# Kernel optimization log

Measured on AMD Instinct MI355X. Metric: run time of the kernel, lower is better.

Reference implementation:

```python
import jax, jax.numpy as jnp
import numpy as np


def _patches3x3(x):
    # x: [B,H,W,C] -> [B,H,W,9,C], SAME zero padding, patch index k = i*3+j
    B, H, W, C = x.shape
    p = jnp.pad(x, ((0, 0), (1, 1), (1, 1), (0, 0)))
    return jnp.stack([p[:, i:i + H, j:j + W, :] for i in range(3) for j in range(3)], axis=3)


def setup_inputs() -> dict:
    key = jax.random.key(0)
    k1, k2, k3 = jax.random.split(key, 3)
    B, H, W, CH, NC, DIM = 4, 80, 80, 256, 22, 256
    x = jax.random.normal(k1, (B, H, W, CH), dtype=jnp.float32)
    seg_mask = jax.random.uniform(k2, (B, H, W, NC), dtype=jnp.float32)
    # he_uniform over receptive field ch*3*3
    lim = np.sqrt(6.0 / (CH * 9)).astype(np.float32)
    conv_w = jax.random.uniform(k3, (CH, 3, 3, DIM), dtype=jnp.float32, minval=-lim, maxval=lim)
    return {"x": x, "seg_mask": seg_mask, "conv_w": conv_w}


def reference(x, seg_mask, conv_w):
    B, H, W, CH = x.shape
    NC = seg_mask.shape[-1]
    DIM = conv_w.shape[-1]
    # patches of segmentation map: [B,H,W,9,NC]
    s_patch = _patches3x3(seg_mask)
    m = seg_mask[:, :, :, None, :]                       # [B,H,W,1,NC]
    s_max = jnp.max(m, axis=-1, keepdims=True)           # [B,H,W,1,1]
    # keep patch values only for the argmax class at the center pixel
    sel = jnp.sum(jnp.where(m == s_max, s_patch, 0.0), axis=-1)  # [B,H,W,9]
    cnt = jnp.sum((sel != 0.0).astype(jnp.float32), axis=-1, keepdims=True)  # [B,H,W,1]
    norm = jnp.where(cnt > 0, 9.0 / jnp.maximum(cnt, 1.0), 0.0)  # divide_no_nan(9, cnt)
    # per-channel 3x3 patch extraction of features (== depthwise conv with eye(9))
    xp = _patches3x3(x)                                  # [B,H,W,9,CH]
    xp = xp * sel[..., None]                             # mask-gated patches
    w = conv_w.reshape(CH, 9, DIM)
    out = jnp.einsum('bhwkc,ckd->bhwd', xp, w) * norm    # [B,H,W,DIM]
    return out
```

## Files before the change

kernel.cpp:

```cpp
#include <hip/hip_runtime.h>
#include <hip/hip_bf16.h>
#include <cstdint>

#define B_ 4
#define H_ 80
#define W_ 80
#define CH_ 256
#define NC_ 22
#define DIM_ 256
#define NPIX (B_*H_*W_)

typedef unsigned short ushort;
typedef __attribute__((ext_vector_type(8))) short short8;
typedef __attribute__((ext_vector_type(4))) float floatx4;

static __device__ inline ushort f2bf(float v) {
    __hip_bfloat16 h = __float2bfloat16(v);
    ushort r;
    __builtin_memcpy(&r, &h, 2);
    return r;
}
static __device__ inline unsigned pk2(float a, float b) {
    return (unsigned)f2bf(a) | ((unsigned)f2bf(b) << 16);
}

__global__ __launch_bounds__(64) void sel_kernel(const float* __restrict__ seg,
                                                 float* __restrict__ ssel)
{
    int m = blockIdx.x * 64 + threadIdx.x;
    if (m >= NPIX) return;
    int w = m % W_;
    int h = (m / W_) % H_;
    int b = m / (W_ * H_);

    const float2* c2 = (const float2*)(seg + (size_t)m * NC_);
    float cv[NC_];
    #pragma unroll
    for (int c = 0; c < NC_ / 2; ++c) { float2 v = c2[c]; cv[2*c] = v.x; cv[2*c+1] = v.y; }
    float mx = -1e30f;
    #pragma unroll
    for (int c = 0; c < NC_; ++c) mx = fmaxf(mx, cv[c]);

    float sel[9];
    int cnt = 0;
    #pragma unroll
    for (int k = 0; k < 9; ++k) {
        int i = k / 3, j = k % 3;
        int hh = h + i - 1, ww = w + j - 1;
        float s = 0.f;
        if (hh >= 0 && hh < H_ && ww >= 0 && ww < W_) {
            const float2* n2 = (const float2*)(seg + ((size_t)((b * H_ + hh) * W_ + ww)) * NC_);
            #pragma unroll
            for (int c = 0; c < NC_ / 2; ++c) {
                float2 v = n2[c];
                s += (cv[2*c]   == mx) ? v.x : 0.f;
                s += (cv[2*c+1] == mx) ? v.y : 0.f;
            }
        }
        sel[k] = s;
        cnt += (s != 0.f) ? 1 : 0;
    }
    float norm = (cnt > 0) ? 9.f / (float)cnt : 0.f;
    #pragma unroll
    for (int k = 0; k < 9; ++k)
        ssel[k * NPIX + m] = sel[k] * norm;
}

__global__ __launch_bounds__(256) void cvt_w(const float* __restrict__ cw,
                                             ushort* __restrict__ wbT)
{
    __shared__ ushort ls[32][260];
    const int k  = blockIdx.x / 8;
    const int c0 = (blockIdx.x % 8) * 32;
    const int c   = threadIdx.x >> 3;
    const int seg = threadIdx.x & 7;

    const float* src = cw + ((size_t)(c0 + c) * 9 + k) * DIM_ + seg * 32;
    #pragma unroll
    for (int e = 0; e < 32; e += 4) {
        float4 v = *(const float4*)(src + e);
        unsigned* dst = (unsigned*)&ls[c][seg * 32 + e];
        dst[0] = pk2(v.x, v.y);
        dst[1] = pk2(v.z, v.w);
    }
    __syncthreads();

    const int d = threadIdx.x;
    ushort tmp[32];
    #pragma unroll
    for (int cc = 0; cc < 32; ++cc) tmp[cc] = ls[cc][d];
    uint4 o[4];
    __builtin_memcpy(o, tmp, 64);
    uint4* dst = (uint4*)(wbT + ((size_t)k * 256 + d) * 256 + c0);
    dst[0] = o[0]; dst[1] = o[1]; dst[2] = o[2]; dst[3] = o[3];
}

__global__ __launch_bounds__(256) void cvt_x(const float* __restrict__ x,
                                             ushort* __restrict__ xb)
{
    size_t idx = ((size_t)blockIdx.x * 256 + threadIdx.x) * 8;
    const float4* s = (const float4*)(x + idx);
    float4 a = s[0], b = s[1];
    uint4 o = make_uint4(pk2(a.x, a.y), pk2(a.z, a.w), pk2(b.x, b.y), pk2(b.z, b.w));
    *(uint4*)(xb + idx) = o;
}

template<bool XB16>
__global__ __launch_bounds__(256, 3) void conv2(const float* __restrict__ x,
                                                const ushort* __restrict__ xb,
                                                const float* __restrict__ ssel,
                                                const ushort* __restrict__ wbT,
                                                float* __restrict__ out)
{
    __shared__ ushort xsA[2][80 * 136];
    __shared__ float  sl[9][80];

    const int tid  = threadIdx.x;
    const int lane = tid & 63;
    const int wv   = tid >> 6;
    const int ln   = lane & 15;
    const int quad = lane >> 4;
    const int rt   = blockIdx.x;
    const int b    = rt / H_;
    const int h    = rt % H_;
    const int d0   = blockIdx.y * 128;

    int qm[5], qc[5];
    #pragma unroll
    for (int r = 0; r < 5; ++r) {
        int q = tid + 256 * r;
        qm[r] = q >> 4;
        qc[r] = q & 15;
    }

    for (int t = tid; t < 9 * 80; t += 256) {
        int k = t / 80, m = t - k * 80;
        sl[k][m] = ssel[k * NPIX + rt * W_ + m];
    }

    floatx4 O[5][2];
    #pragma unroll
    for (int i = 0; i < 5; ++i)
        #pragma unroll
        for (int jn = 0; jn < 2; ++jn)
            O[i][jn] = (floatx4){0.f, 0.f, 0.f, 0.f};

    uint4  sg[5];
    float4 fa[5], fb[5];
    bool   ok[5];

    auto stage_load = [&](int nit) {
        const int i   = nit / 6;
        const int rem = nit % 6;
        const int cc  = (rem / 3) * 128;
        const int jj  = rem % 3;
        const int rr  = h + i - 1;
        const bool rowok = (rr >= 0) && (rr < H_);
        const int rsafe = rowok ? rr : h;
        #pragma unroll
        for (int r = 0; r < 5; ++r) {
            const int col = qm[r] + jj - 1;
            const bool v = rowok && (col >= 0) && (col < W_);
            ok[r] = v;
            const size_t gp = ((size_t)(b * H_ + rsafe) * W_ + (v ? col : 0));
            if (XB16) {
                sg[r] = *(const uint4*)(xb + gp * CH_ + cc + qc[r] * 8);
            } else {
                const float* f = x + gp * CH_ + cc + qc[r] * 8;
                fa[r] = *(const float4*)f;
                fb[r] = *(const float4*)(f + 4);
            }
        }
    };
    auto stage_write = [&](int nit) {
        ushort* bp = xsA[nit & 1];
        #pragma unroll
        for (int r = 0; r < 5; ++r) {
            uint4 v;
            if (XB16) {
                v = ok[r] ? sg[r] : make_uint4(0u, 0u, 0u, 0u);
            } else {
                v = ok[r] ? make_uint4(pk2(fa[r].x, fa[r].y), pk2(fa[r].z, fa[r].w),
                                       pk2(fb[r].x, fb[r].y), pk2(fb[r].z, fb[r].w))
                          : make_uint4(0u, 0u, 0u, 0u);
            }
            *(uint4*)&bp[qm[r] * 136 + qc[r] * 8] = v;
        }
    };

    short8 Breg[8];
    auto loadB = [&](int nit) {
        const int i   = nit / 6;
        const int rem = nit % 6;
        const int cc  = (rem / 3) * 128;
        const int jj  = rem % 3;
        const int k   = 3 * i + jj;
        #pragma unroll
        for (int kk = 0; kk < 4; ++kk)
            #pragma unroll
            for (int jn = 0; jn < 2; ++jn)
                Breg[kk * 2 + jn] = *(const short8*)(wbT
                    + ((size_t)k * 256 + d0 + wv * 32 + jn * 16 + ln) * 256
                    + cc + kk * 32 + quad * 8);
    };

    stage_load(0);
    stage_write(0);
    loadB(0);
    __syncthreads();

    #pragma unroll 2
    for (int it = 0; it < 18; ++it) {
        const int i   = it / 6;
        const int rem = it % 6;
        const int jj  = rem % 3;
        const int k   = 3 * i + jj;
        const ushort* bp = xsA[it & 1];

        if (it < 17) stage_load(it + 1);

        floatx4 P[5][2];
        #pragma unroll
        for (int im = 0; im < 5; ++im)
            #pragma unroll
            for (int jn = 0; jn < 2; ++jn)
                P[im][jn] = (floatx4){0.f, 0.f, 0.f, 0.f};

        #pragma unroll
        for (int kk = 0; kk < 4; ++kk) {
            short8 a[5];
            #pragma unroll
            for (int im = 0; im < 5; ++im)
                a[im] = *(const short8*)&bp[(im * 16 + ln) * 136 + kk * 32 + quad * 8];
            #pragma unroll
            for (int im = 0; im < 5; ++im)
                #pragma unroll
                for (int jn = 0; jn < 2; ++jn)
                    P[im][jn] = __builtin_amdgcn_mfma_f32_16x16x32_bf16(
                        a[im], Breg[kk * 2 + jn], P[im][jn], 0, 0, 0);
        }

        if (it < 17) stage_write(it + 1);
        if (it < 17) loadB(it + 1);

        #pragma unroll
        for (int im = 0; im < 5; ++im) {
            const float4 sv = *(const float4*)&sl[k][im * 16 + quad * 4];
            #pragma unroll
            for (int jn = 0; jn < 2; ++jn) {
                O[im][jn][0] += sv.x * P[im][jn][0];
                O[im][jn][1] += sv.y * P[im][jn][1];
                O[im][jn][2] += sv.z * P[im][jn][2];
                O[im][jn][3] += sv.w * P[im][jn][3];
            }
        }
        __syncthreads();
    }

    #pragma unroll
    for (int im = 0; im < 5; ++im) {
        #pragma unroll
        for (int jn = 0; jn < 2; ++jn) {
            const int dd = d0 + wv * 32 + jn * 16 + ln;
            #pragma unroll
            for (int r = 0; r < 4; ++r) {
                const int m = im * 16 + quad * 4 + r;
                out[((size_t)(rt * W_ + m)) * DIM_ + dd] = O[im][jn][r];
            }
        }
    }
}

extern "C" void kernel_launch(void* const* d_in, const int* in_sizes, int n_in,
                              void* d_out, int out_size, void* d_ws, size_t ws_size,
                              hipStream_t stream)
{
    const float* x   = (const float*)d_in[0];
    const float* seg = (const float*)d_in[1];
    const float* cw  = (const float*)d_in[2];
    float* out = (float*)d_out;

    float*  ssel = (float*)d_ws;
    ushort* wbT  = (ushort*)((char*)d_ws + 921600);
    ushort* xb   = (ushort*)((char*)d_ws + 921600 + 1179648);
    const size_t need = 921600u + 1179648u + 13107200u;

    sel_kernel<<<dim3((NPIX + 63) / 64), dim3(64), 0, stream>>>(seg, ssel);
    cvt_w<<<dim3(72), dim3(256), 0, stream>>>(cw, wbT);

    if (ws_size >= need) {
        cvt_x<<<dim3(NPIX * CH_ / (256 * 8)), dim3(256), 0, stream>>>(x, xb);
        conv2<true><<<dim3(B_ * H_, 2), dim3(256), 0, stream>>>(x, xb, ssel, wbT, out);
    } else {
        conv2<false><<<dim3(B_ * H_, 2), dim3(256), 0, stream>>>(x, nullptr, ssel, wbT, out);
    }
}
```

Measured before the change: 157.4 us.

## Fuse prep kernels, fold selection scale into A staging, retile waves 2x2

The separate sel, weight-convert and x-convert kernels are merged into one prep launch, and sel is now computed per (tap, pixel) thread with normalisation moved into the conv kernel. The conv kernel reads fp32 x directly, multiplies by the per-pixel selection weight while packing to bf16 in LDS, and accumulates straight into the output registers instead of rescaling partial products per tap. Waves are retiled to 2x2 (48 rows by 64 dims each, padded with a zero LDS tile), and B fragments are streamed per k-slice with double buffering. This removes a large bf16 copy of x plus two launches, but scaling before bf16 rounding changes numerics slightly and the padded rows waste some MFMA work.

Result: slower. 198.8 us (+26.2%).

```diff
diff --git a/kernel.cpp b/kernel.cpp
--- a/kernel.cpp
+++ b/kernel.cpp
@@ -24,29 +24,30 @@
     return (unsigned)f2bf(a) | ((unsigned)f2bf(b) << 16);
 }
 
-__global__ __launch_bounds__(64) void sel_kernel(const float* __restrict__ seg,
-                                                 float* __restrict__ ssel)
+__global__ __launch_bounds__(256) void prep(const float* __restrict__ seg,
+                                            const float* __restrict__ cw,
+                                            float* __restrict__ ssel,
+                                            ushort* __restrict__ wbT)
 {
-    int m = blockIdx.x * 64 + threadIdx.x;
-    if (m >= NPIX) return;
-    int w = m % W_;
-    int h = (m / W_) % H_;
-    int b = m / (W_ * H_);
-
-    const float2* c2 = (const float2*)(seg + (size_t)m * NC_);
-    float cv[NC_];
-    #pragma unroll
-    for (int c = 0; c < NC_ / 2; ++c) { float2 v = c2[c]; cv[2*c] = v.x; cv[2*c+1] = v.y; }
-    float mx = -1e30f;
-    #pragma unroll
-    for (int c = 0; c < NC_; ++c) mx = fmaxf(mx, cv[c]);
-
-    float sel[9];
-    int cnt = 0;
-    #pragma unroll
-    for (int k = 0; k < 9; ++k) {
-        int i = k / 3, j = k % 3;
-        int hh = h + i - 1, ww = w + j - 1;
+    __shared__ ushort ls[32][260];
+    if (blockIdx.x < 900) {
+        const int t = blockIdx.x * 256 + threadIdx.x;
+        const int k = t / NPIX;
+        const int m = t - k * NPIX;
+        const int w = m % W_;
+        const int h = (m / W_) % H_;
+        const int b = m / (W_ * H_);
+
+        const float2* c2 = (const float2*)(seg + (size_t)m * NC_);
+        float cv[NC_];
+        #pragma unroll
+        for (int c = 0; c < NC_ / 2; ++c) { float2 v = c2[c]; cv[2*c] = v.x; cv[2*c+1] = v.y; }
+        float mx = -1e30f;
+        #pragma unroll
+        for (int c = 0; c < NC_; ++c) mx = fmaxf(mx, cv[c]);
+
+        const int i = k / 3, j = k % 3;
+        const int hh = h + i - 1, ww = w + j - 1;
         float s = 0.f;
         if (hh >= 0 && hh < H_ && ww >= 0 && ww < W_) {
             const float2* n2 = (const float2*)(seg + ((size_t)((b * H_ + hh) * W_ + ww)) * NC_);
@@ -57,67 +58,49 @@
                 s += (cv[2*c+1] == mx) ? v.y : 0.f;
             }
         }
-        sel[k] = s;
-        cnt += (s != 0.f) ? 1 : 0;
-    }
-    float norm = (cnt > 0) ? 9.f / (float)cnt : 0.f;
-    #pragma unroll
-    for (int k = 0; k < 9; ++k)
-        ssel[k * NPIX + m] = sel[k] * norm;
-}
-
-__global__ __launch_bounds__(256) void cvt_w(const float* __restrict__ cw,
-                                             ushort* __restrict__ wbT)
-{
-    __shared__ ushort ls[32][260];
-    const int k  = blockIdx.x / 8;
-    const int c0 = (blockIdx.x % 8) * 32;
-    const int c   = threadIdx.x >> 3;
-    const int seg = threadIdx.x & 7;
-
-    const float* src = cw + ((size_t)(c0 + c) * 9 + k) * DIM_ + seg * 32;
-    #pragma unroll
-    for (int e = 0; e < 32; e += 4) {
-        float4 v = *(const float4*)(src + e);
-        unsigned* dst = (unsigned*)&ls[c][seg * 32 + e];
-        dst[0] = pk2(v.x, v.y);
-        dst[1] = pk2(v.z, v.w);
-    }
-    __syncthreads();
-
-    const int d = threadIdx.x;
-    ushort tmp[32];
-    #pragma unroll
-    for (int cc = 0; cc < 32; ++cc) tmp[cc] = ls[cc][d];
-    uint4 o[4];
-    __builtin_memcpy(o, tmp, 64);
-    uint4* dst = (uint4*)(wbT + ((size_t)k * 256 + d) * 256 + c0);
-    dst[0] = o[0]; dst[1] = o[1]; dst[2] = o[2]; dst[3] = o[3];
-}
-
-__global__ __launch_bounds__(256) void cvt_x(const float* __restrict__ x,
-                                             ushort* __restrict__ xb)
-{
-    size_t idx = ((size_t)blockIdx.x * 256 + threadIdx.x) * 8;
-    const float4* s = (const float4*)(x + idx);
-    float4 a = s[0], b = s[1];
-    uint4 o = make_uint4(pk2(a.x, a.y), pk2(a.z, a.w), pk2(b.x, b.y), pk2(b.z, b.w));
-    *(uint4*)(xb + idx) = o;
-}
-
-template<bool XB16>
+        ssel[t] = s;
+    } else {
+        const int bx = blockIdx.x - 900;
+        const int k  = bx / 8;
+        const int c0 = (bx % 8) * 32;
+        const int c   = threadIdx.x >> 3;
+        const int seg8 = threadIdx.x & 7;
+
+        const float* src = cw + ((size_t)(c0 + c) * 9 + k) * DIM_ + seg8 * 32;
+        #pragma unroll
+        for (int e = 0; e < 32; e += 4) {
+            float4 v = *(const float4*)(src + e);
+            unsigned* dst = (unsigned*)&ls[c][seg8 * 32 + e];
+            dst[0] = pk2(v.x, v.y);
+            dst[1] = pk2(v.z, v.w);
+        }
+        __syncthreads();
+
+        const int d = threadIdx.x;
+        ushort tmp[32];
+        #pragma unroll
+        for (int cc = 0; cc < 32; ++cc) tmp[cc] = ls[cc][d];
+        uint4 o[4];
+        __builtin_memcpy(o, tmp, 64);
+        uint4* dst = (uint4*)(wbT + ((size_t)k * 256 + d) * 256 + c0);
+        dst[0] = o[0]; dst[1] = o[1]; dst[2] = o[2]; dst[3] = o[3];
+    }
+}
+
 __global__ __launch_bounds__(256, 3) void conv2(const float* __restrict__ x,
-                                                const ushort* __restrict__ xb,
-                                                const float* __restrict__ ssel,
+                                                const float* __restrict__ sraw,
                                                 const ushort* __restrict__ wbT,
                                                 float* __restrict__ out)
 {
     __shared__ ushort xsA[2][80 * 136];
+    __shared__ ushort zs[16 * 136];
     __shared__ float  sl[9][80];
 
     const int tid  = threadIdx.x;
     const int lane = tid & 63;
     const int wv   = tid >> 6;
+    const int wm   = wv >> 1;
+    const int wn   = wv & 1;
     const int ln   = lane & 15;
     const int quad = lane >> 4;
     const int rt   = blockIdx.x;
@@ -125,147 +108,151 @@
     const int h    = rt % H_;
     const int d0   = blockIdx.y * 128;
 
-    int qm[5], qc[5];
+    for (int t2 = tid; t2 < 16 * 136 / 2; t2 += 256) ((unsigned*)zs)[t2] = 0u;
+
+    if (tid < 80) {
+        float raw[9]; int cnt = 0;
+        #pragma unroll
+        for (int k = 0; k < 9; ++k) {
+            raw[k] = sraw[k * NPIX + rt * W_ + tid];
+            cnt += (raw[k] != 0.f) ? 1 : 0;
+        }
+        const float norm = (cnt > 0) ? 9.f / (float)cnt : 0.f;
+        #pragma unroll
+        for (int k = 0; k < 9; ++k) sl[k][tid] = raw[k] * norm;
+    }
+    __syncthreads();
+
+    const int Dbase = (d0 + wn * 64 + ln) * 256 + quad * 8;
+
+    floatx4 O[3][4];
     #pragma unroll
-    for (int r = 0; r < 5; ++r) {
-        int q = tid + 256 * r;
-        qm[r] = q >> 4;
-        qc[r] = q & 15;
-    }
-
-    for (int t = tid; t < 9 * 80; t += 256) {
-        int k = t / 80, m = t - k * 80;
-        sl[k][m] = ssel[k * NPIX + rt * W_ + m];
-    }
-
-    floatx4 O[5][2];
+    for (int im = 0; im < 3; ++im)
+        #pragma unroll
+        for (int jn = 0; jn < 4; ++jn)
+            O[im][jn] = (floatx4){0.f, 0.f, 0.f, 0.f};
+
+    short8 rg[2][4];
+
+    auto loadBn = [&](int itn, int kkn, int slot) {
+        const int ii  = itn / 6;
+        const int rem = itn % 6;
+        const int ccn = (rem / 3) * 128;
+        const int jjn = rem % 3;
+        const int kn  = 3 * ii + jjn;
+        const ushort* bb = wbT + (size_t)kn * 65536 + Dbase + ccn + kkn * 32;
+        #pragma unroll
+        for (int jn = 0; jn < 4; ++jn)
+            rg[slot][jn] = *(const short8*)(bb + jn * 4096);
+    };
+
+    auto stage = [&](int nit) {
+        const int ii  = nit / 6;
+        const int rem = nit % 6;
+        const int ccn = (rem / 3) * 128;
+        const int jjn = rem % 3;
+        const int kn  = 3 * ii + jjn;
+        const int rr  = h + ii - 1;
+        const bool rowok = (rr >= 0) && (rr < H_);
+        ushort* wr = xsA[nit & 1];
+        const float* xrow = x + ((size_t)((b * H_ + (rowok ? rr : 0)) * W_)) * CH_ + ccn;
+        #pragma unroll
+        for (int r = 0; r < 5; ++r) {
+            const int q  = tid + 256 * r;
+            const int qm = q >> 4;
+            const int qc = q & 15;
+            const int col = qm + jjn - 1;
+            const bool v = rowok && (col >= 0) && (col < W_);
+            uint4 o = make_uint4(0u, 0u, 0u, 0u);
+            if (v) {
+                const float s = sl[kn][qm];
+                const float* f = xrow + (size_t)col * CH_ + qc * 8;
+                float4 A  = *(const float4*)f;
+                float4 Bv = *(const float4*)(f + 4);
+                o = make_uint4(pk2(s * A.x, s * A.y), pk2(s * A.z, s * A.w),
+                               pk2(s * Bv.x, s * Bv.y), pk2(s * Bv.z, s * Bv.w));
+            }
+            *(uint4*)&wr[qm * 136 + qc * 8] = o;
+        }
+    };
+
+    stage(0);
+    loadBn(0, 0, 0);
+    __syncthreads();
+
+    for (int it = 0; it < 18; ++it) {
+        const ushort* bp = xsA[it & 1];
+        const ushort* aps[3];
+        #pragma unroll
+        for (int im = 0; im < 3; ++im) {
+            const int row = wm * 48 + im * 16 + ln;
+            aps[im] = ((row < 80) ? (bp + row * 136) : (zs + (row - 80) * 136)) + quad * 8;
+        }
+
+        loadBn(it, 1, 1);
+        {
+            short8 a[3];
+            #pragma unroll
+            for (int im = 0; im < 3; ++im) a[im] = *(const short8*)(aps[im] + 0 * 32);
+            #pragma unroll
+            for (int im = 0; im < 3; ++im)
+                #pragma unroll
+                for (int jn = 0; jn < 4; ++jn)
+                    O[im][jn] = __builtin_amdgcn_mfma_f32_16x16x32_bf16(a[im], rg[0][jn], O[im][jn], 0, 0, 0);
+        }
+
+        if (it < 17) stage(it + 1);
+
+        loadBn(it, 2, 0);
+        {
+            short8 a[3];
+            #pragma unroll
+            for (int im = 0; im < 3; ++im) a[im] = *(const short8*)(aps[im] + 1 * 32);
+            #pragma unroll
+            for (int im = 0; im < 3; ++im)
+                #pragma unroll
+                for (int jn = 0; jn < 4; ++jn)
+                    O[im][jn] = __builtin_amdgcn_mfma_f32_16x16x32_bf16(a[im], rg[1][jn], O[im][jn], 0, 0, 0);
+        }
+
+        loadBn(it, 3, 1);
+        {
+            short8 a[3];
+            #pragma unroll
+            for (int im = 0; im < 3; ++im) a[im] = *(const short8*)(aps[im] + 2 * 32);
+            #pragma unroll
+            for (int im = 0; im < 3; ++im)
+                #pragma unroll
+                for (int jn = 0; jn < 4; ++jn)
+                    O[im][jn] = __builtin_amdgcn_mfma_f32_16x16x32_bf16(a[im], rg[0][jn], O[im][jn], 0, 0, 0);
+        }
+
+        if (it < 17) loadBn(it + 1, 0, 0);
+        {
+            short8 a[3];
+            #pragma unroll
+            for (int im = 0; im < 3; ++im) a[im] = *(const short8*)(aps[im] + 3 * 32);
+            #pragma unroll
+            for (int im = 0; im < 3; ++im)
+                #pragma unroll
+                for (int jn = 0; jn < 4; ++jn)
+                    O[im][jn] = __builtin_amdgcn_mfma_f32_16x16x32_bf16(a[im], rg[1][jn], O[im][jn], 0, 0, 0);
+        }
+
+        __syncthreads();
+    }
+
     #pragma unroll
-    for (int i = 0; i < 5; ++i)
-        #pragma unroll
-        for (int jn = 0; jn < 2; ++jn)
-            O[i][jn] = (floatx4){0.f, 0.f, 0.f, 0.f};
-
-    uint4  sg[5];
-    float4 fa[5], fb[5];
-    bool   ok[5];
-
-    auto stage_load = [&](int nit) {
-        const int i   = nit / 6;
-        const int rem = nit % 6;
-        const int cc  = (rem / 3) * 128;
-        const int jj  = rem % 3;
-        const int rr  = h + i - 1;
-        const bool rowok = (rr >= 0) && (rr < H_);
-        const int rsafe = rowok ? rr : h;
-        #pragma unroll
-        for (int r = 0; r < 5; ++r) {
-            const int col = qm[r] + jj - 1;
-            const bool v = rowok && (col >= 0) && (col < W_);
-            ok[r] = v;
-            const size_t gp = ((size_t)(b * H_ + rsafe) * W_ + (v ? col : 0));
-            if (XB16) {
-                sg[r] = *(const uint4*)(xb + gp * CH_ + cc + qc[r] * 8);
-            } else {
-                const float* f = x + gp * CH_ + cc + qc[r] * 8;
-                fa[r] = *(const float4*)f;
-                fb[r] = *(const float4*)(f + 4);
-            }
-        }
-    };
-    auto stage_write = [&](int nit) {
-        ushort* bp = xsA[nit & 1];
-        #pragma unroll
-        for (int r = 0; r < 5; ++r) {
-            uint4 v;
-            if (XB16) {
-                v = ok[r] ? sg[r] : make_uint4(0u, 0u, 0u, 0u);
-            } else {
-                v = ok[r] ? make_uint4(pk2(fa[r].x, fa[r].y), pk2(fa[r].z, fa[r].w),
-                                       pk2(fb[r].x, fb[r].y), pk2(fb[r].z, fb[r].w))
-                          : make_uint4(0u, 0u, 0u, 0u);
-            }
-            *(uint4*)&bp[qm[r] * 136 + qc[r] * 8] = v;
-        }
-    };
-
-    short8 Breg[8];
-    auto loadB = [&](int nit) {
-        const int i   = nit / 6;
-        const int rem = nit % 6;
-        const int cc  = (rem / 3) * 128;
-        const int jj  = rem % 3;
-        const int k   = 3 * i + jj;
-        #pragma unroll
-        for (int kk = 0; kk < 4; ++kk)
-            #pragma unroll
-            for (int jn = 0; jn < 2; ++jn)
-                Breg[kk * 2 + jn] = *(const short8*)(wbT
-                    + ((size_t)k * 256 + d0 + wv * 32 + jn * 16 + ln) * 256
-                    + cc + kk * 32 + quad * 8);
-    };
-
-    stage_load(0);
-    stage_write(0);
-    loadB(0);
-    __syncthreads();
-
-    #pragma unroll 2
-    for (int it = 0; it < 18; ++it) {
-        const int i   = it / 6;
-        const int rem = it % 6;
-        const int jj  = rem % 3;
-        const int k   = 3 * i + jj;
-        const ushort* bp = xsA[it & 1];
-
-        if (it < 17) stage_load(it + 1);
-
-        floatx4 P[5][2];
-        #pragma unroll
-        for (int im = 0; im < 5; ++im)
-            #pragma unroll
-            for (int jn = 0; jn < 2; ++jn)
-                P[im][jn] = (floatx4){0.f, 0.f, 0.f, 0.f};
-
-        #pragma unroll
-        for (int kk = 0; kk < 4; ++kk) {
-            short8 a[5];
-            #pragma unroll
-            for (int im = 0; im < 5; ++im)
-                a[im] = *(const short8*)&bp[(im * 16 + ln) * 136 + kk * 32 + quad * 8];
-            #pragma unroll
-            for (int im = 0; im < 5; ++im)
-                #pragma unroll
-                for (int jn = 0; jn < 2; ++jn)
-                    P[im][jn] = __builtin_amdgcn_mfma_f32_16x16x32_bf16(
-                        a[im], Breg[kk * 2 + jn], P[im][jn], 0, 0, 0);
-        }
-
-        if (it < 17) stage_write(it + 1);
-        if (it < 17) loadB(it + 1);
-
-        #pragma unroll
-        for (int im = 0; im < 5; ++im) {
-            const float4 sv = *(const float4*)&sl[k][im * 16 + quad * 4];
-            #pragma unroll
-            for (int jn = 0; jn < 2; ++jn) {
-                O[im][jn][0] += sv.x * P[im][jn][0];
-                O[im][jn][1] += sv.y * P[im][jn][1];
-                O[im][jn][2] += sv.z * P[im][jn][2];
-                O[im][jn][3] += sv.w * P[im][jn][3];
-            }
-        }
-        __syncthreads();
-    }
-
-    #pragma unroll
-    for (int im = 0; im < 5; ++im) {
-        #pragma unroll
-        for (int jn = 0; jn < 2; ++jn) {
-            const int dd = d0 + wv * 32 + jn * 16 + ln;
-            #pragma unroll
-            for (int r = 0; r < 4; ++r) {
-                const int m = im * 16 + quad * 4 + r;
-                out[((size_t)(rt * W_ + m)) * DIM_ + dd] = O[im][jn][r];
+    for (int im = 0; im < 3; ++im) {
+        if (!(wm == 1 && im == 2)) {
+            #pragma unroll
+            for (int jn = 0; jn < 4; ++jn) {
+                const int dd = d0 + wn * 64 + jn * 16 + ln;
+                #pragma unroll
+                for (int r = 0; r < 4; ++r) {
+                    const int m = wm * 48 + im * 16 + quad * 4 + r;
+                    out[((size_t)(rt * W_ + m)) * DIM_ + dd] = O[im][jn][r];
+                }
             }
         }
     }
@@ -282,16 +269,7 @@
 
     float*  ssel = (float*)d_ws;
     ushort* wbT  = (ushort*)((char*)d_ws + 921600);
-    ushort* xb   = (ushort*)((char*)d_ws + 921600 + 1179648);
-    const size_t need = 921600u + 1179648u + 13107200u;
-
-    sel_kernel<<<dim3((NPIX + 63) / 64), dim3(64), 0, stream>>>(seg, ssel);
-    cvt_w<<<dim3(72), dim3(256), 0, stream>>>(cw, wbT);
-
-    if (ws_size >= need) {
-        cvt_x<<<dim3(NPIX * CH_ / (256 * 8)), dim3(256), 0, stream>>>(x, xb);
-        conv2<true><<<dim3(B_ * H_, 2), dim3(256), 0, stream>>>(x, xb, ssel, wbT, out);
-    } else {
-        conv2<false><<<dim3(B_ * H_, 2), dim3(256), 0, stream>>>(x, nullptr, ssel, wbT, out);
-    }
-}
+
+    prep<<<dim3(900 + 72), dim3(256), 0, stream>>>(seg, cw, ssel, wbT);
+    conv2<<<dim3(B_ * H_, 2), dim3(256), 0, stream>>>(x, ssel, wbT, out);
+}
```

## Stage full input rows once via direct-to-LDS loads and reuse across horizontal taps

Applied to the files above, without the earlier changes.

The main conv kernel now loads each of the three input rows (82 padded columns by 256 channels, XOR-swizzled) into LDS with global_load_lds. It reuses that one row buffer for all three horizontal taps instead of restaging shifted 128-channel slices 18 times. The selection kernel is spread across 9x more threads (one per pixel-tap), fused with the weight conversion into one launch, and normalisation moves into the conv kernel. In exchange, row staging is no longer double-buffered, so each row load is fenced by two barriers and sits in the critical path.

Result: slower. 264.8 us (+68.2%).

```diff
diff --git a/kernel.cpp b/kernel.cpp
--- a/kernel.cpp
+++ b/kernel.cpp
@@ -14,6 +14,8 @@
 typedef __attribute__((ext_vector_type(8))) short short8;
 typedef __attribute__((ext_vector_type(4))) float floatx4;
 
+__device__ __attribute__((aligned(256))) static const unsigned char zglob[256] = {};
+
 static __device__ inline ushort f2bf(float v) {
     __hip_bfloat16 h = __float2bfloat16(v);
     ushort r;
@@ -23,30 +25,35 @@
 static __device__ inline unsigned pk2(float a, float b) {
     return (unsigned)f2bf(a) | ((unsigned)f2bf(b) << 16);
 }
-
-__global__ __launch_bounds__(64) void sel_kernel(const float* __restrict__ seg,
-                                                 float* __restrict__ ssel)
+static __device__ inline void gll16(const void* g, void* l) {
+    __builtin_amdgcn_global_load_lds((const __attribute__((address_space(1))) void*)g,
+                                     (__attribute__((address_space(3))) void*)l, 16, 0, 0);
+}
+
+__global__ __launch_bounds__(256) void prep(const float* __restrict__ seg,
+                                            const float* __restrict__ cw,
+                                            float* __restrict__ ssel,
+                                            ushort* __restrict__ wbT)
 {
-    int m = blockIdx.x * 64 + threadIdx.x;
-    if (m >= NPIX) return;
-    int w = m % W_;
-    int h = (m / W_) % H_;
-    int b = m / (W_ * H_);
-
-    const float2* c2 = (const float2*)(seg + (size_t)m * NC_);
-    float cv[NC_];
-    #pragma unroll
-    for (int c = 0; c < NC_ / 2; ++c) { float2 v = c2[c]; cv[2*c] = v.x; cv[2*c+1] = v.y; }
-    float mx = -1e30f;
-    #pragma unroll
-    for (int c = 0; c < NC_; ++c) mx = fmaxf(mx, cv[c]);
-
-    float sel[9];
-    int cnt = 0;
-    #pragma unroll
-    for (int k = 0; k < 9; ++k) {
-        int i = k / 3, j = k % 3;
-        int hh = h + i - 1, ww = w + j - 1;
+    __shared__ ushort ls[32][260];
+    if (blockIdx.x < 900) {
+        const int t = blockIdx.x * 256 + threadIdx.x;
+        const int k = t / NPIX;
+        const int m = t - k * NPIX;
+        const int w = m % W_;
+        const int h = (m / W_) % H_;
+        const int b = m / (W_ * H_);
+
+        const float2* c2 = (const float2*)(seg + (size_t)m * NC_);
+        float cv[NC_];
+        #pragma unroll
+        for (int c = 0; c < NC_ / 2; ++c) { float2 v = c2[c]; cv[2*c] = v.x; cv[2*c+1] = v.y; }
+        float mx = -1e30f;
+        #pragma unroll
+        for (int c = 0; c < NC_; ++c) mx = fmaxf(mx, cv[c]);
+
+        const int i = k / 3, j = k % 3;
+        const int hh = h + i - 1, ww = w + j - 1;
         float s = 0.f;
         if (hh >= 0 && hh < H_ && ww >= 0 && ww < W_) {
             const float2* n2 = (const float2*)(seg + ((size_t)((b * H_ + hh) * W_ + ww)) * NC_);
@@ -57,42 +64,33 @@
                 s += (cv[2*c+1] == mx) ? v.y : 0.f;
             }
         }
-        sel[k] = s;
-        cnt += (s != 0.f) ? 1 : 0;
-    }
-    float norm = (cnt > 0) ? 9.f / (float)cnt : 0.f;
-    #pragma unroll
-    for (int k = 0; k < 9; ++k)
-        ssel[k * NPIX + m] = sel[k] * norm;
-}
-
-__global__ __launch_bounds__(256) void cvt_w(const float* __restrict__ cw,
-                                             ushort* __restrict__ wbT)
-{
-    __shared__ ushort ls[32][260];
-    const int k  = blockIdx.x / 8;
-    const int c0 = (blockIdx.x % 8) * 32;
-    const int c   = threadIdx.x >> 3;
-    const int seg = threadIdx.x & 7;
-
-    const float* src = cw + ((size_t)(c0 + c) * 9 + k) * DIM_ + seg * 32;
-    #pragma unroll
-    for (int e = 0; e < 32; e += 4) {
-        float4 v = *(const float4*)(src + e);
-        unsigned* dst = (unsigned*)&ls[c][seg * 32 + e];
-        dst[0] = pk2(v.x, v.y);
-        dst[1] = pk2(v.z, v.w);
-    }
-    __syncthreads();
-
-    const int d = threadIdx.x;
-    ushort tmp[32];
-    #pragma unroll
-    for (int cc = 0; cc < 32; ++cc) tmp[cc] = ls[cc][d];
-    uint4 o[4];
-    __builtin_memcpy(o, tmp, 64);
-    uint4* dst = (uint4*)(wbT + ((size_t)k * 256 + d) * 256 + c0);
-    dst[0] = o[0]; dst[1] = o[1]; dst[2] = o[2]; dst[3] = o[3];
+        ssel[t] = s;
+    } else {
+        const int bx = blockIdx.x - 900;
+        const int k  = bx / 8;
+        const int c0 = (bx % 8) * 32;
+        const int c    = threadIdx.x >> 3;
+        const int seg8 = threadIdx.x & 7;
+
+        const float* src = cw + ((size_t)(c0 + c) * 9 + k) * DIM_ + seg8 * 32;
+        #pragma unroll
+        for (int e = 0; e < 32; e += 4) {
+            float4 v = *(const float4*)(src + e);
+            unsigned* dst = (unsigned*)&ls[c][seg8 * 32 + e];
+            dst[0] = pk2(v.x, v.y);
+            dst[1] = pk2(v.z, v.w);
+        }
+        __syncthreads();
+
+        const int d = threadIdx.x;
+        ushort tmp[32];
+        #pragma unroll
+        for (int cc = 0; cc < 32; ++cc) tmp[cc] = ls[cc][d];
+        uint4 o[4];
+        __builtin_memcpy(o, tmp, 64);
+        uint4* dst = (uint4*)(wbT + ((size_t)k * 256 + d) * 256 + c0);
+        dst[0] = o[0]; dst[1] = o[1]; dst[2] = o[2]; dst[3] = o[3];
+    }
 }
 
 __global__ __launch_bounds__(256) void cvt_x(const float* __restrict__ x,
@@ -105,15 +103,13 @@
     *(uint4*)(xb + idx) = o;
 }
 
-template<bool XB16>
-__global__ __launch_bounds__(256, 3) void conv2(const float* __restrict__ x,
-                                                const ushort* __restrict__ xb,
+__global__ __launch_bounds__(256, 3) void conv2(const ushort* __restrict__ xb,
                                                 const float* __restrict__ ssel,
                                                 const ushort* __restrict__ wbT,
                                                 float* __restrict__ out)
 {
-    __shared__ ushort xsA[2][80 * 136];
-    __shared__ float  sl[9][80];
+    __shared__ __attribute__((aligned(1024))) ushort xt[82 * 32 * 8];
+    __shared__ float sl[9][80];
 
     const int tid  = threadIdx.x;
     const int lane = tid & 63;
@@ -125,18 +121,7 @@
     const int h    = rt % H_;
     const int d0   = blockIdx.y * 128;
 
-    int qm[5], qc[5];
-    #pragma unroll
-    for (int r = 0; r < 5; ++r) {
-        int q = tid + 256 * r;
-        qm[r] = q >> 4;
-        qc[r] = q & 15;
-    }
-
-    for (int t = tid; t < 9 * 80; t += 256) {
-        int k = t / 80, m = t - k * 80;
-        sl[k][m] = ssel[k * NPIX + rt * W_ + m];
-    }
+    const int Dbase = (d0 + wv * 32 + ln) * 256 + quad * 8;
 
     floatx4 O[5][2];
     #pragma unroll
@@ -145,16 +130,191 @@
         for (int jn = 0; jn < 2; ++jn)
             O[i][jn] = (floatx4){0.f, 0.f, 0.f, 0.f};
 
-    uint4  sg[5];
+    short8 rgA[8], rgB[8];
+
+    auto loadBh = [&](int k, int kh, short8* dst) {
+        const ushort* bb = wbT + (size_t)k * 65536 + Dbase + kh * 128;
+        #pragma unroll
+        for (int k2 = 0; k2 < 4; ++k2)
+            #pragma unroll
+            for (int jn = 0; jn < 2; ++jn)
+                dst[k2 * 2 + jn] = *(const short8*)(bb + k2 * 32 + jn * 4096);
+    };
+
+    auto stage_row = [&](int ri) {
+        const int rr = h + ri - 1;
+        const bool rowok = (rr >= 0) && (rr < H_);
+        const ushort* xrow = xb + ((size_t)((b * H_ + (rowok ? rr : 0)) * W_)) * CH_;
+        #pragma unroll
+        for (int n = 0; n < 11; ++n) {
+            const int e = wv + 4 * n;
+            if (e < 41) {
+                const int slot = e * 64 + lane;
+                const int p    = slot >> 5;
+                const int cph  = slot & 31;
+                const int clog = cph ^ (p & 7);
+                const int col  = p - 1;
+                const bool v   = rowok && (col >= 0) && (col < W_);
+                const void* src = v ? (const void*)(xrow + (size_t)col * CH_ + clog * 8)
+                                    : (const void*)zglob;
+                gll16(src, (char*)&xt[0] + e * 1024);
+            }
+        }
+    };
+
+    stage_row(0);
+    loadBh(0, 0, rgA);
+    loadBh(0, 1, rgB);
+    if (tid < 80) {
+        float rv[9]; int cnt = 0;
+        #pragma unroll
+        for (int k = 0; k < 9; ++k) { rv[k] = ssel[k * NPIX + rt * W_ + tid]; cnt += (rv[k] != 0.f) ? 1 : 0; }
+        const float norm = (cnt > 0) ? 9.f / (float)cnt : 0.f;
+        #pragma unroll
+        for (int k = 0; k < 9; ++k) sl[k][tid] = rv[k] * norm;
+    }
+    __syncthreads();
+
+    const floatx4 Z = {0.f, 0.f, 0.f, 0.f};
+    const char* xbase = (const char*)&xt[0];
+
+    for (int t = 0; t < 9; ++t) {
+        const int jj = t - (t / 3) * 3;
+        const int pb = ln + jj;
+        const int sw = pb & 7;
+
+        floatx4 P[3][2];
+
+        #pragma unroll
+        for (int k2 = 0; k2 < 8; ++k2) {
+            const int choff = ((((k2 << 2) | quad) ^ sw) << 4);
+            short8 a0 = *(const short8*)(xbase + (size_t)(pb +  0) * 512 + choff);
+            short8 a1 = *(const short8*)(xbase + (size_t)(pb + 16) * 512 + choff);
+            short8 a2 = *(const short8*)(xbase + (size_t)(pb + 32) * 512 + choff);
+            const short8 b0 = (k2 < 4) ? rgA[k2 * 2 + 0] : rgB[(k2 - 4) * 2 + 0];
+            const short8 b1 = (k2 < 4) ? rgA[k2 * 2 + 1] : rgB[(k2 - 4) * 2 + 1];
+            if (k2 == 0) {
+                P[0][0] = __builtin_amdgcn_mfma_f32_16x16x32_bf16(a0, b0, Z, 0, 0, 0);
+                P[0][1] = __builtin_amdgcn_mfma_f32_16x16x32_bf16(a0, b1, Z, 0, 0, 0);
+                P[1][0] = __builtin_amdgcn_mfma_f32_16x16x32_bf16(a1, b0, Z, 0, 0, 0);
+                P[1][1] = __builtin_amdgcn_mfma_f32_16x16x32_bf16(a1, b1, Z, 0, 0, 0);
+                P[2][0] = __builtin_amdgcn_mfma_f32_16x16x32_bf16(a2, b0, Z, 0, 0, 0);
+                P[2][1] = __builtin_amdgcn_mfma_f32_16x16x32_bf16(a2, b1, Z, 0, 0, 0);
+            } else {
+                P[0][0] = __builtin_amdgcn_mfma_f32_16x16x32_bf16(a0, b0, P[0][0], 0, 0, 0);
+                P[0][1] = __builtin_amdgcn_mfma_f32_16x16x32_bf16(a0, b1, P[0][1], 0, 0, 0);
+                P[1][0] = __builtin_amdgcn_mfma_f32_16x16x32_bf16(a1, b0, P[1][0], 0, 0, 0);
+                P[1][1] = __builtin_amdgcn_mfma_f32_16x16x32_bf16(a1, b1, P[1][1], 0, 0, 0);
+                P[2][0] = __builtin_amdgcn_mfma_f32_16x16x32_bf16(a2, b0, P[2][0], 0, 0, 0);
+                P[2][1] = __builtin_amdgcn_mfma_f32_16x16x32_bf16(a2, b1, P[2][1], 0, 0, 0);
+            }
+        }
+        #pragma unroll
+        for (int im = 0; im < 3; ++im) {
+            const float4 sv = *(const float4*)&sl[t][im * 16 + quad * 4];
+            #pragma unroll
+            for (int jn = 0; jn < 2; ++jn) {
+                O[im][jn][0] += sv.x * P[im][jn][0];
+                O[im][jn][1] += sv.y * P[im][jn][1];
+                O[im][jn][2] += sv.z * P[im][jn][2];
+                O[im][jn][3] += sv.w * P[im][jn][3];
+            }
+        }
+
+        #pragma unroll
+        for (int k2 = 0; k2 < 4; ++k2) {
+            const int choff = ((((k2 << 2) | quad) ^ sw) << 4);
+            short8 a3 = *(const short8*)(xbase + (size_t)(pb + 48) * 512 + choff);
+            short8 a4 = *(const short8*)(xbase + (size_t)(pb + 64) * 512 + choff);
+            if (k2 == 0) {
+                P[0][0] = __builtin_amdgcn_mfma_f32_16x16x32_bf16(a3, rgA[0], Z, 0, 0, 0);
+                P[0][1] = __builtin_amdgcn_mfma_f32_16x16x32_bf16(a3, rgA[1], Z, 0, 0, 0);
+                P[1][0] = __builtin_amdgcn_mfma_f32_16x16x32_bf16(a4, rgA[0], Z, 0, 0, 0);
+                P[1][1] = __builtin_amdgcn_mfma_f32_16x16x32_bf16(a4, rgA[1], Z, 0, 0, 0);
+            } else {
+                P[0][0] = __builtin_amdgcn_mfma_f32_16x16x32_bf16(a3, rgA[k2 * 2 + 0], P[0][0], 0, 0, 0);
+                P[0][1] = __builtin_amdgcn_mfma_f32_16x16x32_bf16(a3, rgA[k2 * 2 + 1], P[0][1], 0, 0, 0);
+                P[1][0] = __builtin_amdgcn_mfma_f32_16x16x32_bf16(a4, rgA[k2 * 2 + 0], P[1][0], 0, 0, 0);
+                P[1][1] = __builtin_amdgcn_mfma_f32_16x16x32_bf16(a4, rgA[k2 * 2 + 1], P[1][1], 0, 0, 0);
+            }
+        }
+        if (t < 8) loadBh(t + 1, 0, rgA);
+        #pragma unroll
+        for (int k2 = 0; k2 < 4; ++k2) {
+            const int choff = (((((k2 + 4) << 2) | quad) ^ sw) << 4);
+            short8 a3 = *(const short8*)(xbase + (size_t)(pb + 48) * 512 + choff);
+            short8 a4 = *(const short8*)(xbase + (size_t)(pb + 64) * 512 + choff);
+            P[0][0] = __builtin_amdgcn_mfma_f32_16x16x32_bf16(a3, rgB[k2 * 2 + 0], P[0][0], 0, 0, 0);
+            P[0][1] = __builtin_amdgcn_mfma_f32_16x16x32_bf16(a3, rgB[k2 * 2 + 1], P[0][1], 0, 0, 0);
+            P[1][0] = __builtin_amdgcn_mfma_f32_16x16x32_bf16(a4, rgB[k2 * 2 + 0], P[1][0], 0, 0, 0);
+            P[1][1] = __builtin_amdgcn_mfma_f32_16x16x32_bf16(a4, rgB[k2 * 2 + 1], P[1][1], 0, 0, 0);
+        }
+        if (t < 8) loadBh(t + 1, 1, rgB);
+        #pragma unroll
+        for (int g = 0; g < 2; ++g) {
+            const float4 sv = *(const float4*)&sl[t][(g + 3) * 16 + quad * 4];
+            #pragma unroll
+            for (int jn = 0; jn < 2; ++jn) {
+                O[g + 3][jn][0] += sv.x * P[g][jn][0];
+                O[g + 3][jn][1] += sv.y * P[g][jn][1];
+                O[g + 3][jn][2] += sv.z * P[g][jn][2];
+                O[g + 3][jn][3] += sv.w * P[g][jn][3];
+            }
+        }
+
+        if (t == 2)      { __syncthreads(); stage_row(1); __syncthreads(); }
+        else if (t == 5) { __syncthreads(); stage_row(2); __syncthreads(); }
+    }
+
+    #pragma unroll
+    for (int im = 0; im < 5; ++im) {
+        #pragma unroll
+        for (int jn = 0; jn < 2; ++jn) {
+            const int dd = d0 + wv * 32 + jn * 16 + ln;
+            #pragma unroll
+            for (int r = 0; r < 4; ++r) {
+                const int m = im * 16 + quad * 4 + r;
+                out[((size_t)(rt * W_ + m)) * DIM_ + dd] = O[im][jn][r];
+            }
+        }
+    }
+}
+
+__global__ __launch_bounds__(256, 3) void conv2_fb(const float* __restrict__ x,
+                                                   const float* __restrict__ ssel,
+                                                   const ushort* __restrict__ wbT,
+                                                   float* __restrict__ out)
+{
+    __shared__ ushort xsA[2][80 * 136];
+    __shared__ float  sl[9][80];
+
+    const int tid  = threadIdx.x;
+    const int lane = tid & 63;
+    const int wv   = tid >> 6;
+    const int ln   = lane & 15;
+    const int quad = lane >> 4;
+    const int rt   = blockIdx.x;
+    const int b    = rt / H_;
+    const int h    = rt % H_;
+    const int d0   = blockIdx.y * 128;
+
+    int qm[5], qc[5];
+    #pragma unroll
+    for (int r = 0; r < 5; ++r) { int q = tid + 256 * r; qm[r] = q >> 4; qc[r] = q & 15; }
+
+    floatx4 O[5][2];
+    #pragma unroll
+    for (int i = 0; i < 5; ++i)
+        #pragma unroll
+        for (int jn = 0; jn < 2; ++jn)
+            O[i][jn] = (floatx4){0.f, 0.f, 0.f, 0.f};
+
     float4 fa[5], fb[5];
     bool   ok[5];
 
     auto stage_load = [&](int nit) {
-        const int i   = nit / 6;
-        const int rem = nit % 6;
-        const int cc  = (rem / 3) * 128;
-        const int jj  = rem % 3;
-        const int rr  = h + i - 1;
+        const int i = nit / 6, rem = nit % 6, cc = (rem / 3) * 128, jj = rem % 3;
+        const int rr = h + i - 1;
         const bool rowok = (rr >= 0) && (rr < H_);
         const int rsafe = rowok ? rr : h;
         #pragma unroll
@@ -162,39 +322,26 @@
             const int col = qm[r] + jj - 1;
             const bool v = rowok && (col >= 0) && (col < W_);
             ok[r] = v;
-            const size_t gp = ((size_t)(b * H_ + rsafe) * W_ + (v ? col : 0));
-            if (XB16) {
-                sg[r] = *(const uint4*)(xb + gp * CH_ + cc + qc[r] * 8);
-            } else {
-                const float* f = x + gp * CH_ + cc + qc[r] * 8;
-                fa[r] = *(const float4*)f;
-                fb[r] = *(const float4*)(f + 4);
-            }
+            const float* f = x + ((size_t)(b * H_ + rsafe) * W_ + (v ? col : 0)) * CH_ + cc + qc[r] * 8;
+            fa[r] = *(const float4*)f;
+            fb[r] = *(const float4*)(f + 4);
         }
     };
     auto stage_write = [&](int nit) {
         ushort* bp = xsA[nit & 1];
         #pragma unroll
         for (int r = 0; r < 5; ++r) {
-            uint4 v;
-            if (XB16) {
-                v = ok[r] ? sg[r] : make_uint4(0u, 0u, 0u, 0u);
-            } else {
-                v = ok[r] ? make_uint4(pk2(fa[r].x, fa[r].y), pk2(fa[r].z, fa[r].w),
-                                       pk2(fb[r].x, fb[r].y), pk2(fb[r].z, fb[r].w))
-                          : make_uint4(0u, 0u, 0u, 0u);
-            }
+            uint4 v = ok[r] ? make_uint4(pk2(fa[r].x, fa[r].y), pk2(fa[r].z, fa[r].w),
+                                         pk2(fb[r].x, fb[r].y), pk2(fb[r].z, fb[r].w))
+                            : make_uint4(0u, 0u, 0u, 0u);
             *(uint4*)&bp[qm[r] * 136 + qc[r] * 8] = v;
         }
     };
 
     short8 Breg[8];
     auto loadB = [&](int nit) {
-        const int i   = nit / 6;
-        const int rem = nit % 6;
-        const int cc  = (rem / 3) * 128;
-        const int jj  = rem % 3;
-        const int k   = 3 * i + jj;
+        const int i = nit / 6, rem = nit % 6, cc = (rem / 3) * 128, jj = rem % 3;
+        const int k = 3 * i + jj;
         #pragma unroll
         for (int kk = 0; kk < 4; ++kk)
             #pragma unroll
@@ -205,16 +352,23 @@
     };
 
     stage_load(0);
+    if (tid < 80) {
+        float rv[9]; int cnt = 0;
+        #pragma unroll
+        for (int k = 0; k < 9; ++k) { rv[k] = ssel[k * NPIX + rt * W_ + tid]; cnt += (rv[k] != 0.f) ? 1 : 0; }
+        const float norm = (cnt > 0) ? 9.f / (float)cnt : 0.f;
+        #pragma unroll
+        for (int k = 0; k < 9; ++k) sl[k][tid] = rv[k] * norm;
+    }
+    __syncthreads();
     stage_write(0);
     loadB(0);
     __syncthreads();
 
     #pragma unroll 2
     for (int it = 0; it < 18; ++it) {
-        const int i   = it / 6;
-        const int rem = it % 6;
-        const int jj  = rem % 3;
-        const int k   = 3 * i + jj;
+        const int i = it / 6, rem = it % 6, jj = rem % 3;
+        const int k = 3 * i + jj;
         const ushort* bp = xsA[it & 1];
 
         if (it < 17) stage_load(it + 1);
@@ -258,7 +412,7 @@
     }
 
     #pragma unroll
-    for (int im = 0; im < 5; ++im) {
+    for (int im = 0; im < 5; ++im)
         #pragma unroll
         for (int jn = 0; jn < 2; ++jn) {
             const int dd = d0 + wv * 32 + jn * 16 + ln;
@@ -268,7 +422,6 @@
                 out[((size_t)(rt * W_ + m)) * DIM_ + dd] = O[im][jn][r];
             }
         }
-    }
 }
 
 extern "C" void kernel_launch(void* const* d_in, const int* in_sizes, int n_in,
@@ -285,13 +438,12 @@
     ushort* xb   = (ushort*)((char*)d_ws + 921600 + 1179648);
     const size_t need = 921600u + 1179648u + 13107200u;
 
-    sel_kernel<<<dim3((NPIX + 63) / 64), dim3(64), 0, stream>>>(seg, ssel);
-    cvt_w<<<dim3(72), dim3(256), 0, stream>>>(cw, wbT);
+    prep<<<dim3(900 + 72), dim3(256), 0, stream>>>(seg, cw, ssel, wbT);
 
     if (ws_size >= need) {
         cvt_x<<<dim3(NPIX * CH_ / (256 * 8)), dim3(256), 0, stream>>>(x, xb);
-        conv2<true><<<dim3(B_ * H_, 2), dim3(256), 0, stream>>>(x, xb, ssel, wbT, out);
+        conv2<<<dim3(B_ * H_, 2), dim3(256), 0, stream>>>(xb, ssel, wbT, out);
     } else {
-        conv2<false><<<dim3(B_ * H_, 2), dim3(256), 0, stream>>>(x, nullptr, ssel, wbT, out);
-    }
-}
+        conv2_fb<<<dim3(B_ * H_, 2), dim3(256), 0, stream>>>(x, ssel, wbT, out);
+    }
+}
```

## Merge sel, weight and x conversion kernels into one prep launch

Applied to the files above, without the earlier changes.

Combines the three preprocessing kernels into a single launch that branches on block index, cutting two kernel launches and their serialization gaps. The selection work is split so each thread computes one (tap, pixel) pair, which adds parallelism. The count-based normalization moves into the conv kernel's shared-memory staging, overlapping with the first tile load. The cost is that each of the nine tap threads per pixel re-reads the centre pixel's segmentation row to find its max, and the conv prologue does slightly more work.

Result: no change. 156.4 us (-0.7%).

```diff
diff --git a/kernel.cpp b/kernel.cpp
--- a/kernel.cpp
+++ b/kernel.cpp
@@ -24,29 +24,32 @@
     return (unsigned)f2bf(a) | ((unsigned)f2bf(b) << 16);
 }
 
-__global__ __launch_bounds__(64) void sel_kernel(const float* __restrict__ seg,
-                                                 float* __restrict__ ssel)
+__global__ __launch_bounds__(256) void prep(const float* __restrict__ seg,
+                                            const float* __restrict__ cw,
+                                            const float* __restrict__ x,
+                                            float* __restrict__ ssel,
+                                            ushort* __restrict__ wbT,
+                                            ushort* __restrict__ xb)
 {
-    int m = blockIdx.x * 64 + threadIdx.x;
-    if (m >= NPIX) return;
-    int w = m % W_;
-    int h = (m / W_) % H_;
-    int b = m / (W_ * H_);
-
-    const float2* c2 = (const float2*)(seg + (size_t)m * NC_);
-    float cv[NC_];
-    #pragma unroll
-    for (int c = 0; c < NC_ / 2; ++c) { float2 v = c2[c]; cv[2*c] = v.x; cv[2*c+1] = v.y; }
-    float mx = -1e30f;
-    #pragma unroll
-    for (int c = 0; c < NC_; ++c) mx = fmaxf(mx, cv[c]);
-
-    float sel[9];
-    int cnt = 0;
-    #pragma unroll
-    for (int k = 0; k < 9; ++k) {
-        int i = k / 3, j = k % 3;
-        int hh = h + i - 1, ww = w + j - 1;
+    __shared__ ushort ls[32][260];
+    if (blockIdx.x < 900) {
+        const int t = blockIdx.x * 256 + threadIdx.x;
+        const int k = t / NPIX;
+        const int m = t - k * NPIX;
+        const int w = m % W_;
+        const int h = (m / W_) % H_;
+        const int b = m / (W_ * H_);
+
+        const float2* c2 = (const float2*)(seg + (size_t)m * NC_);
+        float cv[NC_];
+        #pragma unroll
+        for (int c = 0; c < NC_ / 2; ++c) { float2 v = c2[c]; cv[2*c] = v.x; cv[2*c+1] = v.y; }
+        float mx = -1e30f;
+        #pragma unroll
+        for (int c = 0; c < NC_; ++c) mx = fmaxf(mx, cv[c]);
+
+        const int i = k / 3, j = k % 3;
+        const int hh = h + i - 1, ww = w + j - 1;
         float s = 0.f;
         if (hh >= 0 && hh < H_ && ww >= 0 && ww < W_) {
             const float2* n2 = (const float2*)(seg + ((size_t)((b * H_ + hh) * W_ + ww)) * NC_);
@@ -57,52 +60,39 @@
                 s += (cv[2*c+1] == mx) ? v.y : 0.f;
             }
         }
-        sel[k] = s;
-        cnt += (s != 0.f) ? 1 : 0;
-    }
-    float norm = (cnt > 0) ? 9.f / (float)cnt : 0.f;
-    #pragma unroll
-    for (int k = 0; k < 9; ++k)
-        ssel[k * NPIX + m] = sel[k] * norm;
-}
-
-__global__ __launch_bounds__(256) void cvt_w(const float* __restrict__ cw,
-                                             ushort* __restrict__ wbT)
-{
-    __shared__ ushort ls[32][260];
-    const int k  = blockIdx.x / 8;
-    const int c0 = (blockIdx.x % 8) * 32;
-    const int c   = threadIdx.x >> 3;
-    const int seg = threadIdx.x & 7;
-
-    const float* src = cw + ((size_t)(c0 + c) * 9 + k) * DIM_ + seg * 32;
-    #pragma unroll
-    for (int e = 0; e < 32; e += 4) {
-        float4 v = *(const float4*)(src + e);
-        unsigned* dst = (unsigned*)&ls[c][seg * 32 + e];
-        dst[0] = pk2(v.x, v.y);
-        dst[1] = pk2(v.z, v.w);
-    }
-    __syncthreads();
-
-    const int d = threadIdx.x;
-    ushort tmp[32];
-    #pragma unroll
-    for (int cc = 0; cc < 32; ++cc) tmp[cc] = ls[cc][d];
-    uint4 o[4];
-    __builtin_memcpy(o, tmp, 64);
-    uint4* dst = (uint4*)(wbT + ((size_t)k * 256 + d) * 256 + c0);
-    dst[0] = o[0]; dst[1] = o[1]; dst[2] = o[2]; dst[3] = o[3];
-}
-
-__global__ __launch_bounds__(256) void cvt_x(const float* __restrict__ x,
-                                             ushort* __restrict__ xb)
-{
-    size_t idx = ((size_t)blockIdx.x * 256 + threadIdx.x) * 8;
-    const float4* s = (const float4*)(x + idx);
-    float4 a = s[0], b = s[1];
-    uint4 o = make_uint4(pk2(a.x, a.y), pk2(a.z, a.w), pk2(b.x, b.y), pk2(b.z, b.w));
-    *(uint4*)(xb + idx) = o;
+        ssel[t] = s;
+    } else if (blockIdx.x < 972) {
+        const int bx = blockIdx.x - 900;
+        const int k  = bx / 8;
+        const int c0 = (bx % 8) * 32;
+        const int c    = threadIdx.x >> 3;
+        const int seg8 = threadIdx.x & 7;
+
+        const float* src = cw + ((size_t)(c0 + c) * 9 + k) * DIM_ + seg8 * 32;
+        #pragma unroll
+        for (int e = 0; e < 32; e += 4) {
+            float4 v = *(const float4*)(src + e);
+            unsigned* dst = (unsigned*)&ls[c][seg8 * 32 + e];
+            dst[0] = pk2(v.x, v.y);
+            dst[1] = pk2(v.z, v.w);
+        }
+        __syncthreads();
+
+        const int d = threadIdx.x;
+        ushort tmp[32];
+        #pragma unroll
+        for (int cc = 0; cc < 32; ++cc) tmp[cc] = ls[cc][d];
+        uint4 o[4];
+        __builtin_memcpy(o, tmp, 64);
+        uint4* dst = (uint4*)(wbT + ((size_t)k * 256 + d) * 256 + c0);
+        dst[0] = o[0]; dst[1] = o[1]; dst[2] = o[2]; dst[3] = o[3];
+    } else if (xb != nullptr) {
+        size_t idx = ((size_t)(blockIdx.x - 972) * 256 + threadIdx.x) * 8;
+        const float4* s = (const float4*)(x + idx);
+        float4 a = s[0], b = s[1];
+        uint4 o = make_uint4(pk2(a.x, a.y), pk2(a.z, a.w), pk2(b.x, b.y), pk2(b.z, b.w));
+        *(uint4*)(xb + idx) = o;
+    }
 }
 
 template<bool XB16>
@@ -131,11 +121,6 @@
         int q = tid + 256 * r;
         qm[r] = q >> 4;
         qc[r] = q & 15;
-    }
-
-    for (int t = tid; t < 9 * 80; t += 256) {
-        int k = t / 80, m = t - k * 80;
-        sl[k][m] = ssel[k * NPIX + rt * W_ + m];
     }
 
     floatx4 O[5][2];
@@ -205,6 +190,17 @@
     };
 
     stage_load(0);
+    if (tid < 80) {
+        float rv[9]; int cnt = 0;
+        #pragma unroll
+        for (int k = 0; k < 9; ++k) {
+            rv[k] = ssel[k * NPIX + rt * W_ + tid];
+            cnt += (rv[k] != 0.f) ? 1 : 0;
+        }
+        const float norm = (cnt > 0) ? 9.f / (float)cnt : 0.f;
+        #pragma unroll
+        for (int k = 0; k < 9; ++k) sl[k][tid] = rv[k] * norm;
+    }
     stage_write(0);
     loadB(0);
     __syncthreads();
@@ -285,13 +281,11 @@
     ushort* xb   = (ushort*)((char*)d_ws + 921600 + 1179648);
     const size_t need = 921600u + 1179648u + 13107200u;
 
-    sel_kernel<<<dim3((NPIX + 63) / 64), dim3(64), 0, stream>>>(seg, ssel);
-    cvt_w<<<dim3(72), dim3(256), 0, stream>>>(cw, wbT);
-
     if (ws_size >= need) {
-        cvt_x<<<dim3(NPIX * CH_ / (256 * 8)), dim3(256), 0, stream>>>(x, xb);
+        prep<<<dim3(972 + 3200), dim3(256), 0, stream>>>(seg, cw, x, ssel, wbT, xb);
         conv2<true><<<dim3(B_ * H_, 2), dim3(256), 0, stream>>>(x, xb, ssel, wbT, out);
     } else {
+        prep<<<dim3(972), dim3(256), 0, stream>>>(seg, cw, x, ssel, wbT, nullptr);
         conv2<false><<<dim3(B_ * H_, 2), dim3(256), 0, stream>>>(x, nullptr, ssel, wbT, out);
     }
 }
```
